# Kernel tuning notes

Measured on AMD Instinct MI355X. Metric: run time of the kernel, lower is better.

The kernel has to match this reference:

```python
import jax, jax.numpy as jnp
import numpy as np

D_MODEL = 2048
D_COMPARE = 2048
D_MEMORY = 2048
N_HEADS = 16
KV_HEADS = 4
KV_REPEAT = N_HEADS // KV_HEADS          # 4
C_HD = D_COMPARE // N_HEADS              # 128 compare head dim
M_HD = D_MEMORY // N_HEADS               # 128 memory head dim
TOTAL_OUT = D_COMPARE + KV_HEADS * C_HD + KV_HEADS * M_HD  # 3072


def setup_inputs() -> dict:
    key = jax.random.key(0)
    ks = jax.random.split(key, 5)
    b, t = 2, 2048
    x = jax.random.normal(ks[0], (b, t, D_MODEL), dtype=jnp.float32)
    s_in = 1.0 / np.sqrt(D_MODEL)
    s_out = 1.0 / np.sqrt(D_MEMORY)
    in_w = jax.random.uniform(ks[1], (TOTAL_OUT, D_MODEL), jnp.float32, -s_in, s_in)
    in_b = jax.random.uniform(ks[2], (TOTAL_OUT,), jnp.float32, -s_in, s_in)
    out_w = jax.random.uniform(ks[3], (D_MODEL, D_MEMORY), jnp.float32, -s_out, s_out)
    out_b = jax.random.uniform(ks[4], (D_MODEL,), jnp.float32, -s_out, s_out)
    return {"x": x, "in_w": in_w, "in_b": in_b, "out_w": out_w, "out_b": out_b}


def reference(x, in_w, in_b, out_w, out_b):
    b, t, _ = x.shape
    packed = jnp.einsum("btd,od->bto", x, in_w) + in_b          # [b,t,TOTAL_OUT]
    q, k, v = jnp.split(packed, [D_COMPARE, D_COMPARE + KV_HEADS * C_HD], axis=-1)
    # q: [b, kv, rep, t, hd] -- head h maps to kv group h // KV_REPEAT
    # (torch repeat_interleave on KV head dim == grouped reshape of q heads)
    q = q.reshape(b, t, KV_HEADS, KV_REPEAT, C_HD).transpose(0, 2, 3, 1, 4)
    k = k.reshape(b, t, KV_HEADS, C_HD).transpose(0, 2, 1, 3)   # [b,kv,t,hd]
    v = v.reshape(b, t, KV_HEADS, M_HD).transpose(0, 2, 1, 3)   # [b,kv,t,mhd]
    scale = 1.0 / np.sqrt(C_HD)
    scores = jnp.einsum("bgrqd,bgkd->bgrqk", q, k) * scale      # [b,kv,rep,t,t]
    attn = jax.nn.softmax(scores, axis=-1)
    y = jnp.einsum("bgrqk,bgkd->bgrqd", attn, v)                # [b,kv,rep,t,mhd]
    y = y.transpose(0, 3, 1, 2, 4).reshape(b, t, D_MEMORY)      # heads back in order
    return jnp.einsum("btm,dm->btd", y, out_w) + out_b
```

## Files before the change

kernel.cpp:

```cpp
#include <hip/hip_runtime.h>
#include <hip/hip_bf16.h>
#include <stdint.h>

#define DEV __device__ __forceinline__

typedef __attribute__((ext_vector_type(8))) short bf16x8;
typedef __attribute__((ext_vector_type(4))) float f32x4;
typedef __attribute__((ext_vector_type(16))) float f32x16;
typedef __attribute__((ext_vector_type(4))) unsigned u32x4;

DEV unsigned short f2bf(float f) {
  unsigned u = __builtin_bit_cast(unsigned, f);
  unsigned r = u + 0x7FFF + ((u >> 16) & 1);
  return (unsigned short)(r >> 16);
}

DEV unsigned short f2bfh(float f) {
  __bf16 h = (__bf16)f;
  return __builtin_bit_cast(unsigned short, h);
}

DEV unsigned cvtpk(float lo, float hi) {
  unsigned r;
  asm("v_cvt_pk_bf16_f32 %0, %1, %2" : "=v"(r) : "v"(lo), "v"(hi));
  return r;
}

DEV void plswap(unsigned &a, unsigned &b) {
  asm("v_permlane32_swap_b32 %0, %1" : "+v"(a), "+v"(b));
}

typedef __attribute__((address_space(1))) void gvoid;
typedef __attribute__((address_space(3))) void lvoid;

DEV void g2l16(const void* g, void* l) {
  __builtin_amdgcn_global_load_lds((gvoid*)g, (lvoid*)l, 16, 0, 0);
}

#define MFMA16(a, b, c) __builtin_amdgcn_mfma_f32_16x16x32_bf16(a, b, c, 0, 0, 0)
#define MFMA32(a, b, c) __builtin_amdgcn_mfma_f32_32x32x16_bf16(a, b, c, 0, 0, 0)

__global__ void k_cvt3(const float* __restrict__ x, unsigned short* __restrict__ xo, int nx4,
                       const float* __restrict__ w, unsigned short* __restrict__ wo, int nw4,
                       const float* __restrict__ v, unsigned short* __restrict__ vo, int nv4) {
  int i = blockIdx.x * blockDim.x + threadIdx.x;
  int stride = gridDim.x * blockDim.x;
  int tot = nx4 + nw4 + nv4;
  for (; i < tot; i += stride) {
    const float* src; unsigned short* dst; int j = i;
    if (j < nx4) { src = x; dst = xo; }
    else if ((j -= nx4) < nw4) { src = w; dst = wo; }
    else { j -= nw4; src = v; dst = vo; }
    float4 val = reinterpret_cast<const float4*>(src)[j];
    ushort4 o;
    o.x = f2bf(val.x); o.y = f2bf(val.y); o.z = f2bf(val.z); o.w = f2bf(val.w);
    reinterpret_cast<ushort4*>(dst)[j] = o;
  }
}

template<bool BF16OUT>
__global__ __launch_bounds__(256, 2) void k_gemm(
    const unsigned short* __restrict__ A, const unsigned short* __restrict__ B,
    const float* __restrict__ bias, void* __restrict__ C,
    int M, int N, int K) {
  __shared__ unsigned short As[128 * 32];
  __shared__ unsigned short Bs[128 * 32];
  int tid = threadIdx.x;
  int lane = tid & 63, wid = tid >> 6;
  int bm = blockIdx.y * 128, bn = blockIdx.x * 128;
  int wm = (wid >> 1) * 64, wn = (wid & 1) * 64;
  int row16 = lane & 15, kq = lane >> 4;
  f32x4 acc[4][4] = {};
  int r = tid >> 2, c = (tid & 3) * 8;
  const unsigned short* Ag = A + (size_t)(bm + r) * K + c;
  const unsigned short* Bg = B + (size_t)(bn + r) * K + c;
  for (int k0 = 0; k0 < K; k0 += 32) {
    g2l16(Ag + k0, &As[tid * 8]);
    g2l16(Ag + (size_t)64 * K + k0, &As[2048 + tid * 8]);
    g2l16(Bg + k0, &Bs[tid * 8]);
    g2l16(Bg + (size_t)64 * K + k0, &Bs[2048 + tid * 8]);
    __syncthreads();
    bf16x8 a[4], b[4];
#pragma unroll
    for (int m = 0; m < 4; m++) a[m] = *(const bf16x8*)&As[(wm + m * 16 + row16) * 32 + kq * 8];
#pragma unroll
    for (int n = 0; n < 4; n++) b[n] = *(const bf16x8*)&Bs[(wn + n * 16 + row16) * 32 + kq * 8];
    __builtin_amdgcn_s_setprio(1);
#pragma unroll
    for (int m = 0; m < 4; m++)
#pragma unroll
      for (int n = 0; n < 4; n++)
        acc[m][n] = MFMA16(a[m], b[n], acc[m][n]);
    __builtin_amdgcn_s_setprio(0);
    __syncthreads();
  }
#pragma unroll
  for (int n = 0; n < 4; n++) {
    int col = bn + wn + n * 16 + row16;
    float bv = bias[col];
#pragma unroll
    for (int m = 0; m < 4; m++) {
      int rw = bm + wm + m * 16 + kq * 4;
#pragma unroll
      for (int j = 0; j < 4; j++) {
        float v = acc[m][n][j] + bv;
        if (BF16OUT) ((unsigned short*)C)[(size_t)(rw + j) * N + col] = f2bf(v);
        else         ((float*)C)[(size_t)(rw + j) * N + col] = v;
      }
    }
  }
}

__global__ void k_pack(const unsigned short* __restrict__ packed, unsigned short* __restrict__ attp) {
  __shared__ unsigned short tile[64][136];
  int t = blockIdx.x, g = blockIdx.y;
  int b = g >> 2, kv = g & 3;
  int tid = threadIdx.x;
#pragma unroll
  for (int i = 0; i < 4; i++) {
    int tl = i * 16 + (tid >> 4);
    int d0 = (tid & 15) * 8;
    *(bf16x8*)&tile[tl][d0] =
        *(const bf16x8*)&packed[(size_t)(b * 2048 + t * 64 + tl) * 3072 + 2560 + kv * 128 + d0];
  }
  size_t obase = (size_t)(g * 32 + t) * 32 * 64 * 8;
#pragma unroll
  for (int f = 0; f < 4; f++) {
    int idx = f * 256 + tid;
    int frag = idx >> 6, lane = idx & 63;
    int l31 = lane & 31, h2 = lane >> 5;
    int kb2 = frag >> 3, kc = frag & 7;
    const unsigned short* src = &packed[(size_t)(b * 2048 + t * 64 + kb2 * 32 + l31) * 3072
                                        + 2048 + kv * 128 + (2 * kc + h2) * 8];
    *(bf16x8*)&attp[obase + (size_t)(frag * 64 + lane) * 8] = *(const bf16x8*)src;
  }
  __syncthreads();
#pragma unroll
  for (int f = 0; f < 4; f++) {
    int idx = f * 256 + tid;
    int f16 = idx >> 6, lane = idx & 63;
    int l31 = lane & 31, h2 = lane >> 5;
    int db = f16 >> 2, ks = f16 & 3;
    int d = 32 * db + l31;
    bf16x8 ov;
#pragma unroll
    for (int e = 0; e < 8; e++) ov[e] = (short)tile[(2 * ks + h2) * 8 + e][d];
    *(bf16x8*)&attp[obase + (size_t)((16 + f16) * 64 + lane) * 8] = ov;
  }
}

__global__ __launch_bounds__(512, 1) void k_flashS(
    const unsigned short* __restrict__ packed,
    const unsigned short* __restrict__ attp,
    unsigned short* __restrict__ Y) {
  __shared__ unsigned short S[4][16384];
  int tid = threadIdx.x, lane = tid & 63, wid = tid >> 6;
  int l31 = lane & 31, hi = lane >> 5;
  int kx = l31 & 15;
  int g = blockIdx.x;
  int s8 = g & 7;
  int b = s8 >> 2, kv = s8 & 3;
  int w = g >> 3;
  int h = kv * 4 + (w & 3);
  int qt = w >> 2;
  size_t prow = (size_t)b * 2048;

  unsigned short* Sf = &S[0][0];
  {
    int rr = tid >> 4;
    int cc = ((tid & 15) ^ (rr & 15)) * 8;
    const unsigned short* qg = packed + (prow + qt * 256 + rr) * 3072 + h * 128 + cc;
#pragma unroll
    for (int i = 0; i < 8; i++)
      g2l16(qg + (size_t)i * 32 * 3072, &Sf[i * 4096 + tid * 8]);
  }
  asm volatile("s_waitcnt vmcnt(0)" ::: "memory");
  __builtin_amdgcn_s_barrier();
  bf16x8 q[8];
  int qrow = wid * 32 + l31;
#pragma unroll
  for (int kc = 0; kc < 8; kc++)
    q[kc] = *(const bf16x8*)&Sf[qrow * 128 + (((2 * kc + hi) ^ kx) * 8)];
  asm volatile("s_waitcnt lgkmcnt(0)" ::: "memory");
  __builtin_amdgcn_sched_barrier(0);
  __builtin_amdgcn_s_barrier();

  const unsigned short* tstr = attp + (size_t)s8 * 32 * 16384;

  auto stage = [&](int t, int buf) {
    const unsigned short* src = tstr + (size_t)t * 16384 + tid * 8;
    unsigned short* dst = &S[buf][tid * 8];
#pragma unroll
    for (int i = 0; i < 4; i++)
      g2l16(src + i * 4096, dst + i * 4096);
  };

  auto qk = [&](int buf, f32x16& s0, f32x16& s1) {
    const unsigned short* B = &S[buf][0];
    bf16x8 ak[4];
#pragma unroll
    for (int j = 0; j < 4; j++) ak[j] = *(const bf16x8*)&B[((0 + j) * 64 + lane) * 8];
    __builtin_amdgcn_s_setprio(1);
#pragma unroll
    for (int j = 0; j < 4; j++) s0 = MFMA32(ak[j], q[j], s0);
    __builtin_amdgcn_s_setprio(0);
#pragma unroll
    for (int j = 0; j < 4; j++) ak[j] = *(const bf16x8*)&B[((4 + j) * 64 + lane) * 8];
    __builtin_amdgcn_s_setprio(1);
#pragma unroll
    for (int j = 0; j < 4; j++) s0 = MFMA32(ak[j], q[4 + j], s0);
    __builtin_amdgcn_s_setprio(0);
#pragma unroll
    for (int j = 0; j < 4; j++) ak[j] = *(const bf16x8*)&B[((8 + j) * 64 + lane) * 8];
    __builtin_amdgcn_s_setprio(1);
#pragma unroll
    for (int j = 0; j < 4; j++) s1 = MFMA32(ak[j], q[j], s1);
    __builtin_amdgcn_s_setprio(0);
#pragma unroll
    for (int j = 0; j < 4; j++) ak[j] = *(const bf16x8*)&B[((12 + j) * 64 + lane) * 8];
    __builtin_amdgcn_s_setprio(1);
#pragma unroll
    for (int j = 0; j < 4; j++) s1 = MFMA32(ak[j], q[4 + j], s1);
    __builtin_amdgcn_s_setprio(0);
  };

  const float sc2 = 0.08838834764831845f * 1.4426950408889634f;
  const float MOFF = 14.f;

  auto smcvt = [&](f32x16& a0, f32x16& a1, bf16x8* pf) {
#pragma unroll
    for (int r = 0; r < 16; r++) a0[r] = exp2f(fmaf(a0[r], sc2, -MOFF));
#pragma unroll
    for (int r = 0; r < 16; r++) a1[r] = exp2f(fmaf(a1[r], sc2, -MOFF));
    unsigned E0 = cvtpk(a0[0],  a0[1]);
    unsigned E1 = cvtpk(a0[2],  a0[3]);
    unsigned E2 = cvtpk(a0[4],  a0[5]);
    unsigned E3 = cvtpk(a0[6],  a0[7]);
    unsigned E4 = cvtpk(a0[8],  a0[9]);
    unsigned E5 = cvtpk(a0[10], a0[11]);
    unsigned E6 = cvtpk(a0[12], a0[13]);
    unsigned E7 = cvtpk(a0[14], a0[15]);
    plswap(E0, E2); plswap(E1, E3);
    plswap(E4, E6); plswap(E5, E7);
    pf[0] = __builtin_bit_cast(bf16x8, u32x4{E0, E1, E2, E3});
    pf[1] = __builtin_bit_cast(bf16x8, u32x4{E4, E5, E6, E7});
    unsigned F0 = cvtpk(a1[0],  a1[1]);
    unsigned F1 = cvtpk(a1[2],  a1[3]);
    unsigned F2 = cvtpk(a1[4],  a1[5]);
    unsigned F3 = cvtpk(a1[6],  a1[7]);
    unsigned F4 = cvtpk(a1[8],  a1[9]);
    unsigned F5 = cvtpk(a1[10], a1[11]);
    unsigned F6 = cvtpk(a1[12], a1[13]);
    unsigned F7 = cvtpk(a1[14], a1[15]);
    plswap(F0, F2); plswap(F1, F3);
    plswap(F4, F6); plswap(F5, F7);
    pf[2] = __builtin_bit_cast(bf16x8, u32x4{F0, F1, F2, F3});
    pf[3] = __builtin_bit_cast(bf16x8, u32x4{F4, F5, F6, F7});
  };

  f32x16 o[4] = {};
  f32x16 ls = {};
  bf16x8 ones;
#pragma unroll
  for (int e = 0; e < 8; e++) ones[e] = (short)0x3F80;

  auto pv = [&](int buf, bf16x8* pf) {
#pragma unroll
    for (int ks = 0; ks < 4; ks++) ls = MFMA32(pf[ks], ones, ls);
    const unsigned short* B = &S[buf][0];
#pragma unroll
    for (int db = 0; db < 4; db++) {
      bf16x8 bv[4];
#pragma unroll
      for (int ks = 0; ks < 4; ks++)
        bv[ks] = *(const bf16x8*)&B[((16 + db * 4 + ks) * 64 + lane) * 8];
      __builtin_amdgcn_s_setprio(1);
#pragma unroll
      for (int ks = 0; ks < 4; ks++) o[db] = MFMA32(pf[ks], bv[ks], o[db]);
      __builtin_amdgcn_s_setprio(0);
    }
  };

  stage(0, 0);
  stage(1, 1);
  asm volatile("s_waitcnt vmcnt(0)" ::: "memory");
  __builtin_amdgcn_s_barrier();

  bool isA = wid < 4;
  f32x16 stc0 = {}, stc1 = {};
  bf16x8 pfB[4];
  if (isA) qk(0, stc0, stc1);

  for (int t = 0; t < 32; t++) {
    int tn2 = t + 2 <= 31 ? t + 2 : 31;
    stage(tn2, (t + 2) & 3);

    if (isA) {
      f32x16 sn0 = {}, sn1 = {};
      qk((t + 1) & 3, sn0, sn1);
      bf16x8 pfA[4];
      smcvt(stc0, stc1, pfA);
      pv(t & 3, pfA);
      stc0 = sn0;
      stc1 = sn1;
    } else {
      if (t > 0) pv((t - 1) & 3, pfB);
      f32x16 sb0 = {}, sb1 = {};
      qk(t & 3, sb0, sb1);
      smcvt(sb0, sb1, pfB);
    }

    asm volatile("s_waitcnt vmcnt(0)" ::: "memory");
    __builtin_amdgcn_s_barrier();
  }
  if (!isA) pv(3, pfB);

#pragma unroll
  for (int r = 0; r < 16; r++) {
    int ql = (r & 3) + 8 * (r >> 2) + 4 * hi;
    float inv = 1.f / ls[r];
    size_t orow = prow + (size_t)qt * 256 + wid * 32 + ql;
#pragma unroll
    for (int db = 0; db < 4; db++)
      Y[orow * 2048 + h * 128 + db * 32 + l31] = f2bfh(o[db][r] * inv);
  }
}

extern "C" void kernel_launch(void* const* d_in, const int* in_sizes, int n_in,
                              void* d_out, int out_size, void* d_ws, size_t ws_size,
                              hipStream_t stream) {
  const float* x     = (const float*)d_in[0];
  const float* in_w  = (const float*)d_in[1];
  const float* in_b  = (const float*)d_in[2];
  const float* out_w = (const float*)d_in[3];
  const float* out_b = (const float*)d_in[4];
  float* out = (float*)d_out;

  unsigned short* xb     = (unsigned short*)d_ws;
  unsigned short* wb     = xb + 8388608;
  unsigned short* owb    = wb + 6291456;
  unsigned short* packed = owb + 4194304;
  unsigned short* y      = packed + 12582912;
  unsigned short* attp   = xb;

  k_cvt3<<<dim3(2048), dim3(256), 0, stream>>>(x, xb, 8388608 / 4,
                                               in_w, wb, 6291456 / 4,
                                               out_w, owb, 4194304 / 4);

  k_gemm<true><<<dim3(24, 32), dim3(256), 0, stream>>>(xb, wb, in_b, packed, 4096, 3072, 2048);
  k_pack<<<dim3(32, 8), dim3(256), 0, stream>>>(packed, attp);
  k_flashS<<<dim3(256), dim3(512), 0, stream>>>(packed, attp, y);
  k_gemm<false><<<dim3(16, 32), dim3(256), 0, stream>>>(y, owb, out_b, out, 4096, 2048, 2048);
}
```

Before: 213.8 us.

## Double GEMM K-tile to 64 and XOR-swizzle LDS layout

The projection GEMM now stages a 64-wide K slice per iteration instead of 32, which halves the number of barrier-separated iterations and doubles the MFMAs issued between syncs. The LDS rows are XOR-swizzled on 16-byte chunks, on both the global-to-LDS writes and the fragment reads, to avoid bank conflicts from the wider row stride. LDS use per block doubles and more fragment registers are live, which may reduce occupancy under the 2-blocks-per-CU launch bound.

```diff
diff --git a/kernel.cpp b/kernel.cpp
--- a/kernel.cpp
+++ b/kernel.cpp
@@ -63,34 +63,49 @@
     const unsigned short* __restrict__ A, const unsigned short* __restrict__ B,
     const float* __restrict__ bias, void* __restrict__ C,
     int M, int N, int K) {
-  __shared__ unsigned short As[128 * 32];
-  __shared__ unsigned short Bs[128 * 32];
+  __shared__ unsigned short As[128 * 64];
+  __shared__ unsigned short Bs[128 * 64];
   int tid = threadIdx.x;
   int lane = tid & 63, wid = tid >> 6;
   int bm = blockIdx.y * 128, bn = blockIdx.x * 128;
   int wm = (wid >> 1) * 64, wn = (wid & 1) * 64;
   int row16 = lane & 15, kq = lane >> 4;
+  int s7 = row16 & 7;
   f32x4 acc[4][4] = {};
-  int r = tid >> 2, c = (tid & 3) * 8;
-  const unsigned short* Ag = A + (size_t)(bm + r) * K + c;
-  const unsigned short* Bg = B + (size_t)(bn + r) * K + c;
-  for (int k0 = 0; k0 < K; k0 += 32) {
-    g2l16(Ag + k0, &As[tid * 8]);
-    g2l16(Ag + (size_t)64 * K + k0, &As[2048 + tid * 8]);
-    g2l16(Bg + k0, &Bs[tid * 8]);
-    g2l16(Bg + (size_t)64 * K + k0, &Bs[2048 + tid * 8]);
+  int r = tid >> 3;
+  int cS = ((tid & 7) ^ (r & 7)) * 8;
+  const unsigned short* Ag = A + (size_t)(bm + r) * K + cS;
+  const unsigned short* Bg = B + (size_t)(bn + r) * K + cS;
+  for (int k0 = 0; k0 < K; k0 += 64) {
+#pragma unroll
+    for (int i = 0; i < 4; i++) {
+      g2l16(Ag + (size_t)i * 32 * K + k0, &As[i * 2048 + tid * 8]);
+      g2l16(Bg + (size_t)i * 32 * K + k0, &Bs[i * 2048 + tid * 8]);
+    }
     __syncthreads();
-    bf16x8 a[4], b[4];
-#pragma unroll
-    for (int m = 0; m < 4; m++) a[m] = *(const bf16x8*)&As[(wm + m * 16 + row16) * 32 + kq * 8];
-#pragma unroll
-    for (int n = 0; n < 4; n++) b[n] = *(const bf16x8*)&Bs[(wn + n * 16 + row16) * 32 + kq * 8];
-    __builtin_amdgcn_s_setprio(1);
-#pragma unroll
-    for (int m = 0; m < 4; m++)
-#pragma unroll
-      for (int n = 0; n < 4; n++)
-        acc[m][n] = MFMA16(a[m], b[n], acc[m][n]);
+    bf16x8 a[4][2], b[4][2];
+#pragma unroll
+    for (int m = 0; m < 4; m++) {
+      int row = wm + m * 16 + row16;
+#pragma unroll
+      for (int kb = 0; kb < 2; kb++)
+        a[m][kb] = *(const bf16x8*)&As[row * 64 + (((kb * 4 + kq) ^ s7) * 8)];
+    }
+#pragma unroll
+    for (int n = 0; n < 4; n++) {
+      int row = wn + n * 16 + row16;
+#pragma unroll
+      for (int kb = 0; kb < 2; kb++)
+        b[n][kb] = *(const bf16x8*)&Bs[row * 64 + (((kb * 4 + kq) ^ s7) * 8)];
+    }
+    __builtin_amdgcn_s_setprio(1);
+#pragma unroll
+    for (int kb = 0; kb < 2; kb++)
+#pragma unroll
+      for (int m = 0; m < 4; m++)
+#pragma unroll
+        for (int n = 0; n < 4; n++)
+          acc[m][n] = MFMA16(a[m][kb], b[n][kb], acc[m][n]);
     __builtin_amdgcn_s_setprio(0);
     __syncthreads();
   }
```

Measured after the change: 198.1 us, median of 2. 7.3% less time.
